# Optimization experiments

Measured on AMD Instinct MI355X. Metric: run time of the kernel, lower is better.

Reference implementation:

```python
import jax, jax.numpy as jnp
import numpy as np

NEURON_CDECAY = 0.5
NEURON_VDECAY = 0.75
NEURON_VTH = 0.5
SPIKE_PSEUDO_GRAD_WINDOW = 0.5

@jax.custom_vjp
def pseudo_spike(v):
    return (v > NEURON_VTH).astype(v.dtype)

def _ps_fwd(v):
    return pseudo_spike(v), v

def _ps_bwd(v, g):
    return (g * (jnp.abs(v - NEURON_VTH) < SPIKE_PSEUDO_GRAD_WINDOW).astype(g.dtype),)

pseudo_spike.defvjp(_ps_fwd, _ps_bwd)

def conv1d(x, w, b):
    # x: (B, Cin, L), w: (Cout, Cin, K), stride 2, VALID padding
    y = jax.lax.conv_general_dilated(x, w, window_strides=(2,), padding='VALID',
                                     dimension_numbers=('NCH', 'OIH', 'NCH'))
    return y + b[None, :, None]

def neuron(syn_out, u, v, s):
    u = u * NEURON_CDECAY + syn_out
    v = v * NEURON_VDECAY * (1.0 - s) + u
    s = pseudo_spike(v)
    return u, v, s

def setup_inputs() -> dict:
    key = jax.random.key(0)
    ks = jax.random.split(key, 18)
    B, T, L = 4096, 50, 360
    h1, h2, h3, A = 256, 256, 128, 2
    def w(k, shape, fan_in):
        bound = 1.0 / np.sqrt(fan_in)
        return jax.random.uniform(k, shape, jnp.float32, -bound, bound)
    return {
        'normal_spikes': (jax.random.uniform(ks[0], (B, 6, T)) < 0.5).astype(jnp.float32),
        'scan_spikes': (jax.random.uniform(ks[1], (B, 1, L, T)) < 0.5).astype(jnp.float32),
        'batch_size': B,
        'conv1_w': w(ks[2], (5, 1, 5), 5),   'conv1_b': w(ks[3], (5,), 5),
        'conv2_w': w(ks[4], (5, 5, 5), 25),  'conv2_b': w(ks[5], (5,), 25),
        'conv3_w': w(ks[6], (5, 5, 5), 25),  'conv3_b': w(ks[7], (5,), 25),
        'fc1_w': w(ks[8], (h1, 216), 216),   'fc1_b': w(ks[9], (h1,), 216),
        'fc2_w': w(ks[10], (h2, h1), h1),    'fc2_b': w(ks[11], (h2,), h1),
        'fc3_w': w(ks[12], (h3, h2), h2),    'fc3_b': w(ks[13], (h3,), h2),
        'fc4_w': w(ks[14], (A, h3), h3),     'fc4_b': w(ks[15], (A,), h3),
    }

def reference(normal_spikes, scan_spikes, batch_size,
              conv1_w, conv1_b, conv2_w, conv2_b, conv3_w, conv3_b,
              fc1_w, fc1_b, fc2_w, fc2_b, fc3_w, fc3_b, fc4_w, fc4_b):
    B = batch_size
    T = normal_spikes.shape[-1]
    A = fc4_w.shape[0]
    # time-major sequences for lax.scan
    scan_seq = jnp.moveaxis(scan_spikes, -1, 0)    # (T, B, 1, 360)
    norm_seq = jnp.moveaxis(normal_spikes, -1, 0)  # (T, B, 6)

    z = lambda *s: jnp.zeros(s, jnp.float32)
    init = (
        (z(B, 5, 178), z(B, 5, 178), z(B, 5, 178)),
        (z(B, 5, 87),  z(B, 5, 87),  z(B, 5, 87)),
        (z(B, 5, 42),  z(B, 5, 42),  z(B, 5, 42)),
        (z(B, 256), z(B, 256), z(B, 256)),
        (z(B, 256), z(B, 256), z(B, 256)),
        (z(B, 128), z(B, 128), z(B, 128)),
        (z(B, A),   z(B, A),   z(B, A)),
        z(B, A),
    )

    def step(carry, xs):
        c1, c2, c3, f1, f2, f3, f4, acc = carry
        scan_x, norm_x = xs
        c1 = neuron(conv1d(scan_x, conv1_w, conv1_b), *c1)
        c2 = neuron(conv1d(c1[2], conv2_w, conv2_b), *c2)
        c3 = neuron(conv1d(c2[2], conv3_w, conv3_b), *c3)
        comb = jnp.concatenate([c3[2].reshape(B, -1), norm_x], axis=1)  # (B, 216)
        f1 = neuron(comb @ fc1_w.T + fc1_b, *f1)
        f2 = neuron(f1[2] @ fc2_w.T + fc2_b, *f2)
        f3 = neuron(f2[2] @ fc3_w.T + fc3_b, *f3)
        f4 = neuron(f3[2] @ fc4_w.T + fc4_b, *f4)
        acc = acc + f4[2]
        return (c1, c2, c3, f1, f2, f3, f4, acc), None

    carry, _ = jax.lax.scan(step, init, (scan_seq, norm_seq))
    return carry[-1] / T
```

## Files before the change

### kernel.cpp

```cpp
#include <hip/hip_runtime.h>
#include <cstdint>
#include <cstddef>


#define NB 4096
#define MTOT (NB * 50)

typedef __attribute__((ext_vector_type(2))) float f32x2;

__device__ __forceinline__ void neuron_update(float syn, float& u, float& v, float& s) {
    u = u * 0.5f + syn;
    v = v * 0.75f * (1.0f - s) + u;
    s = (v > 0.5f) ? 1.0f : 0.0f;
}

__global__ __launch_bounds__(192) void conv1_kernel(
    const float* __restrict__ x, const float* __restrict__ w1,
    const float* __restrict__ b1, unsigned long long* __restrict__ S1)
{
    __shared__ float xl[9000];
    const int tid = threadIdx.x;
    const int b = blockIdx.x;
    const int j = tid;
    const int lbase = (j < 178) ? 2 * j : 354;

    float wr[25], br[5];
#pragma unroll
    for (int q = 0; q < 25; ++q) wr[q] = w1[q];
#pragma unroll
    for (int o = 0; o < 5; ++o) br[o] = b1[o];

    float u[5], v[5], s[5];
#pragma unroll
    for (int o = 0; o < 5; ++o) { u[o] = 0.f; v[o] = 0.f; s[o] = 0.f; }

    const float* xb = x + (size_t)b * 18000;
    for (int half = 0; half < 2; ++half) {
        const int t0 = half * 25;
        __syncthreads();
        for (int e = tid; e < 9000; e += 192)
            xl[e] = xb[(e / 25) * 50 + t0 + (e % 25)];
        __syncthreads();
        for (int dt = 0; dt < 25; ++dt) {
            const int t = t0 + dt;
            float xv[5];
#pragma unroll
            for (int k = 0; k < 5; ++k) xv[k] = xl[(lbase + k) * 25 + dt];
#pragma unroll
            for (int o = 0; o < 5; ++o) {
                float syn = 0.f;
#pragma unroll
                for (int k = 0; k < 5; ++k) syn += wr[o * 5 + k] * xv[k];
                syn += br[o];
                neuron_update(syn, u[o], v[o], s[o]);
                unsigned long long m = __ballot(j < 178 && s[o] > 0.5f);
                if ((tid & 63) == 0)
                    S1[(((size_t)b * 50 + t) * 5 + o) * 3 + (tid >> 6)] = m;
            }
        }
    }
}

__global__ __launch_bounds__(128) void conv2_kernel(
    const unsigned int* __restrict__ S1, const float* __restrict__ w2,
    const float* __restrict__ b2, unsigned int* __restrict__ S2)
{
    __shared__ unsigned int s1l[1501];
    const int tid = threadIdx.x;
    const int b = blockIdx.x;

    float wr[125], br[5];
#pragma unroll
    for (int q = 0; q < 125; ++q) wr[q] = w2[q];
#pragma unroll
    for (int o = 0; o < 5; ++o) br[o] = b2[o];

    const unsigned int* src = S1 + (size_t)b * 1500;
    for (int e = tid; e < 1500; e += 128) s1l[e] = src[e];
    __syncthreads();

    const int p = (tid < 87) ? 2 * tid : 172;
    const int pw = p >> 5, ps = p & 31;

    float u[5], v[5], s[5];
#pragma unroll
    for (int o = 0; o < 5; ++o) { u[o] = 0.f; v[o] = 0.f; s[o] = 0.f; }

    for (int t = 0; t < 50; ++t) {
        float xv[25];
#pragma unroll
        for (int ci = 0; ci < 5; ++ci) {
            const int base = (t * 5 + ci) * 6 + pw;
            unsigned long long bits =
                ((((unsigned long long)s1l[base + 1]) << 32) | (unsigned long long)s1l[base]) >> ps;
#pragma unroll
            for (int k = 0; k < 5; ++k)
                xv[ci * 5 + k] = ((bits >> k) & 1ULL) ? 1.0f : 0.0f;
        }
#pragma unroll
        for (int o = 0; o < 5; ++o) {
            float syn = 0.f;
#pragma unroll
            for (int q = 0; q < 25; ++q) syn += wr[o * 25 + q] * xv[q];
            syn += br[o];
            neuron_update(syn, u[o], v[o], s[o]);
            unsigned long long m = __ballot(tid < 87 && s[o] > 0.5f);
            const size_t outb = (((size_t)b * 50 + t) * 5 + o) * 3;
            if (tid == 0) {
                S2[outb]     = (unsigned int)m;
                S2[outb + 1] = (unsigned int)(m >> 32);
            }
            if (tid == 64) S2[outb + 2] = (unsigned int)m;
        }
    }
}

__global__ __launch_bounds__(64) void conv3_kernel(
    const unsigned int* __restrict__ S2, const float* __restrict__ w3,
    const float* __restrict__ b3, const float* __restrict__ normal,
    unsigned int* __restrict__ ST0)
{
    __shared__ unsigned int s2l[751];
    const int tid = threadIdx.x;
    const int b = blockIdx.x;

    float wr[125], br[5];
#pragma unroll
    for (int q = 0; q < 125; ++q) wr[q] = w3[q];
#pragma unroll
    for (int o = 0; o < 5; ++o) br[o] = b3[o];

    const unsigned int* src = S2 + (size_t)b * 750;
    for (int e = tid; e < 750; e += 64) s2l[e] = src[e];
    __syncthreads();

    const int p = (tid < 42) ? 2 * tid : 82;
    const int pw = p >> 5, ps = p & 31;

    float u[5], v[5], s[5];
#pragma unroll
    for (int o = 0; o < 5; ++o) { u[o] = 0.f; v[o] = 0.f; s[o] = 0.f; }

    for (int t = 0; t < 50; ++t) {
        float xv[25];
#pragma unroll
        for (int ci = 0; ci < 5; ++ci) {
            const int base = (t * 5 + ci) * 3 + pw;
            unsigned long long bits =
                ((((unsigned long long)s2l[base + 1]) << 32) | (unsigned long long)s2l[base]) >> ps;
#pragma unroll
            for (int k = 0; k < 5; ++k)
                xv[ci * 5 + k] = ((bits >> k) & 1ULL) ? 1.0f : 0.0f;
        }
        unsigned long long m[5];
#pragma unroll
        for (int o = 0; o < 5; ++o) {
            float syn = 0.f;
#pragma unroll
            for (int q = 0; q < 25; ++q) syn += wr[o * 25 + q] * xv[q];
            syn += br[o];
            neuron_update(syn, u[o], v[o], s[o]);
            m[o] = __ballot(tid < 42 && s[o] > 0.5f);
        }
        const unsigned long long nm =
            __ballot(tid < 6 && normal[((size_t)b * 6 + tid) * 50 + t] > 0.5f);
        if (tid == 0) {
            const unsigned long long r0 = m[0] | (m[1] << 42);
            const unsigned long long r1 = (m[1] >> 22) | (m[2] << 20) | (m[3] << 62);
            const unsigned long long r2 = (m[3] >> 2) | (m[4] << 40);
            const unsigned long long r3 = (m[4] >> 24) | (nm << 18);
            const size_t mrow = (size_t)b * 50 + t;
            ST0[0 * (size_t)MTOT + mrow] = (unsigned int)r0;
            ST0[1 * (size_t)MTOT + mrow] = (unsigned int)(r0 >> 32);
            ST0[2 * (size_t)MTOT + mrow] = (unsigned int)r1;
            ST0[3 * (size_t)MTOT + mrow] = (unsigned int)(r1 >> 32);
            ST0[4 * (size_t)MTOT + mrow] = (unsigned int)r2;
            ST0[5 * (size_t)MTOT + mrow] = (unsigned int)(r2 >> 32);
            ST0[6 * (size_t)MTOT + mrow] = (unsigned int)r3;
        }
    }
}

__global__ __launch_bounds__(256) void transpose_w_kernel(
    const float* __restrict__ W, float* __restrict__ Wt, int N, int KREAL, int KPAD)
{
    const int idx = blockIdx.x * 256 + threadIdx.x;
    if (idx >= KPAD * N) return;
    const int k = idx / N, n = idx % N;
    Wt[idx] = (k < KREAL) ? W[(size_t)n * KREAL + k] : 0.f;
}

template <int NTOT, int KT>
__global__ __launch_bounds__(256, 2) void pk_gemm_kernel(
    const uint32_t* __restrict__ bitsT,
    const float* __restrict__ Wt,
    const float* __restrict__ bias,
    float* __restrict__ syn,
    int row0)
{
    __shared__ __align__(16) float blds[2][32 * 128];

    const int tid = threadIdx.x;
    const int lane = tid & 63;
    const int wid = tid >> 6;
    const int tm = tid & 15;
    const int tn = tid >> 4;
    const int m0 = blockIdx.x * 256;
    const int nbase = blockIdx.y * 128;

    auto stage = [&](int kt, int buf) {
#pragma unroll
        for (int j = 0; j < 4; ++j) {
            const int c = (j * 4 + wid) * 64 + lane;
            const int row = c >> 5, col = c & 31;
            const float* src = Wt + (size_t)(kt * 32 + row) * NTOT + nbase + col * 4;
            float* dst = &blds[buf][0] + (size_t)(j * 4 + wid) * 256 + lane * 4;
            __builtin_amdgcn_global_load_lds(
                (const __attribute__((address_space(1))) uint32_t*)src,
                (__attribute__((address_space(3))) uint32_t*)dst, 16, 0, 0);
        }
    };

    const int rowA = row0 + m0 + tm * 16;
    auto loadA = [&](int kt, uint4& q0, uint4& q1, uint4& q2, uint4& q3) {
        const uint32_t* p = bitsT + (size_t)kt * MTOT + rowA;
        q0 = *reinterpret_cast<const uint4*>(p);
        q1 = *reinterpret_cast<const uint4*>(p + 4);
        q2 = *reinterpret_cast<const uint4*>(p + 8);
        q3 = *reinterpret_cast<const uint4*>(p + 12);
    };

    uint4 A0, A1, A2, A3, N0, N1, N2, N3;
    loadA(0, A0, A1, A2, A3);
    stage(0, 0);

    f32x2 acc[16][4];
#pragma unroll
    for (int mi = 0; mi < 16; ++mi)
#pragma unroll
        for (int r2 = 0; r2 < 4; ++r2) acc[mi][r2] = (f32x2){0.f, 0.f};

    for (int kt = 0; kt < KT; ++kt) {
        __syncthreads();
        if (kt + 1 < KT) {
            stage(kt + 1, (kt + 1) & 1);
            loadA(kt + 1, N0, N1, N2, N3);
        }

        uint awv[16] = {A0.x, A0.y, A0.z, A0.w, A1.x, A1.y, A1.z, A1.w,
                        A2.x, A2.y, A2.z, A2.w, A3.x, A3.y, A3.z, A3.w};
        const float* bt = &blds[kt & 1][0];

#pragma unroll
        for (int kk = 0; kk < 32; ++kk) {
            f32x2 w2[4];
#pragma unroll
            for (int r2 = 0; r2 < 4; ++r2)
                w2[r2] = *reinterpret_cast<const f32x2*>(bt + kk * 128 + tn * 8 + r2 * 2);
            f32x2 av = {0.f, 0.f};
#pragma unroll
            for (int mi = 0; mi < 16; ++mi) {
                av.x = (float)((awv[mi] >> kk) & 1u);
#pragma unroll
                for (int r2 = 0; r2 < 4; ++r2)
                    asm("v_pk_fma_f32 %0, %1, %2, %0 op_sel_hi:[0,1,1]"
                        : "+v"(acc[mi][r2]) : "v"(av), "v"(w2[r2]));
            }
        }
        if (kt + 1 < KT) { A0 = N0; A1 = N1; A2 = N2; A3 = N3; }
    }

    const int nb = nbase + tn * 8;
    float bsv[8];
#pragma unroll
    for (int q = 0; q < 8; ++q) bsv[q] = bias[nb + q];
#pragma unroll
    for (int mi = 0; mi < 16; ++mi) {
        float* so = syn + (size_t)(m0 + tm * 16 + mi) * NTOT + nb;
        float4 o0, o1;
        o0.x = acc[mi][0].x + bsv[0]; o0.y = acc[mi][0].y + bsv[1];
        o0.z = acc[mi][1].x + bsv[2]; o0.w = acc[mi][1].y + bsv[3];
        o1.x = acc[mi][2].x + bsv[4]; o1.y = acc[mi][2].y + bsv[5];
        o1.z = acc[mi][3].x + bsv[6]; o1.w = acc[mi][3].y + bsv[7];
        *reinterpret_cast<float4*>(so) = o0;
        *reinterpret_cast<float4*>(so + 4) = o1;
    }
}

__global__ __launch_bounds__(256) void fc_scanT_kernel(
    const float* __restrict__ syn, uint32_t* __restrict__ SFT, int b0)
{
    const int tid = threadIdx.x;
    const int lane = tid & 63;
    const int ob = tid >> 6;
    const int bl = blockIdx.x;
    const int o = ob * 64 + lane;

    float u = 0.f, v = 0.f, s = 0.f;
    for (int t = 0; t < 50; ++t) {
        const float sv = syn[((size_t)bl * 50 + t) * 256 + o];
        neuron_update(sv, u, v, s);
        const unsigned long long m = __ballot(s > 0.5f);
        if (lane == 0) {
            const size_t row = (size_t)(b0 + bl) * 50 + t;
            SFT[(size_t)(2 * ob) * MTOT + row]     = (uint32_t)m;
            SFT[(size_t)(2 * ob + 1) * MTOT + row] = (uint32_t)(m >> 32);
        }
    }
}

__global__ __launch_bounds__(256) void fc_scan128_kernel(
    const float* __restrict__ syn, unsigned long long* __restrict__ SF, int b0)
{
    const int tid = threadIdx.x;
    const int wid = blockIdx.x * 4 + (tid >> 6);
    const int lane = tid & 63;
    const int bl = wid >> 1;
    const int ob = wid & 1;
    const int o = ob * 64 + lane;

    float u = 0.f, v = 0.f, s = 0.f;
    for (int t = 0; t < 50; ++t) {
        const float sv = syn[((size_t)bl * 50 + t) * 128 + o];
        neuron_update(sv, u, v, s);
        const unsigned long long m = __ballot(s > 0.5f);
        if (lane == 0) SF[((size_t)(b0 + bl) * 50 + t) * 2 + ob] = m;
    }
}

__global__ __launch_bounds__(256) void fc4_gemm_kernel(
    const unsigned long long* __restrict__ SF3, const float* __restrict__ W,
    const float* __restrict__ bias, float* __restrict__ syn4)
{
    const int m = blockIdx.x * 256 + threadIdx.x;
    const unsigned long long w0 = SF3[(size_t)m * 2];
    const unsigned long long w1 = SF3[(size_t)m * 2 + 1];
    float a0 = 0.f, a1 = 0.f;
#pragma unroll
    for (int i = 0; i < 64; ++i) {
        const float bit = ((w0 >> i) & 1ULL) ? 1.f : 0.f;
        a0 = fmaf(bit, W[i], a0);
        a1 = fmaf(bit, W[128 + i], a1);
    }
#pragma unroll
    for (int i = 0; i < 64; ++i) {
        const float bit = ((w1 >> i) & 1ULL) ? 1.f : 0.f;
        a0 = fmaf(bit, W[64 + i], a0);
        a1 = fmaf(bit, W[192 + i], a1);
    }
    syn4[(size_t)m * 2]     = a0 + bias[0];
    syn4[(size_t)m * 2 + 1] = a1 + bias[1];
}

__global__ __launch_bounds__(64) void fc4_scan_kernel(
    const float* __restrict__ syn4, float* __restrict__ out)
{
    const int b = blockIdx.x * 64 + threadIdx.x;
    float u0 = 0.f, v0 = 0.f, s0 = 0.f, acc0 = 0.f;
    float u1 = 0.f, v1 = 0.f, s1 = 0.f, acc1 = 0.f;
    for (int t = 0; t < 50; ++t) {
        const float x0 = syn4[((size_t)b * 50 + t) * 2];
        const float x1 = syn4[((size_t)b * 50 + t) * 2 + 1];
        neuron_update(x0, u0, v0, s0); acc0 += s0;
        neuron_update(x1, u1, v1, s1); acc1 += s1;
    }
    out[b * 2]     = acc0 / 50.0f;
    out[b * 2 + 1] = acc1 / 50.0f;
}

extern "C" void kernel_launch(void* const* d_in, const int* in_sizes, int n_in,
                              void* d_out, int out_size, void* d_ws, size_t ws_size,
                              hipStream_t stream) {
    (void)in_sizes; (void)n_in; (void)out_size;
    const float* normal = (const float*)d_in[0];
    const float* xscan  = (const float*)d_in[1];
    const float* w1  = (const float*)d_in[3];
    const float* b1  = (const float*)d_in[4];
    const float* w2  = (const float*)d_in[5];
    const float* b2  = (const float*)d_in[6];
    const float* w3  = (const float*)d_in[7];
    const float* b3  = (const float*)d_in[8];
    const float* fw1 = (const float*)d_in[9];
    const float* fb1 = (const float*)d_in[10];
    const float* fw2 = (const float*)d_in[11];
    const float* fb2 = (const float*)d_in[12];
    const float* fw3 = (const float*)d_in[13];
    const float* fb3 = (const float*)d_in[14];
    const float* fw4 = (const float*)d_in[15];
    const float* fb4 = (const float*)d_in[16];
    float* out = (float*)d_out;

    char* wp = (char*)d_ws;
    size_t off = 0;
    auto take = [&](size_t bytes) -> void* {
        void* p = wp + off;
        off += (bytes + 255) & ~(size_t)255;
        return p;
    };
    float* Wt1 = (float*)take((size_t)224 * 256 * 4);
    float* Wt2 = (float*)take((size_t)256 * 256 * 4);
    float* Wt3 = (float*)take((size_t)256 * 128 * 4);
    unsigned long long* S1  = (unsigned long long*)take((size_t)NB * 50 * 15 * 8);
    unsigned int*       S2  = (unsigned int*)take((size_t)NB * 50 * 15 * 4);
    uint32_t* ST0 = (uint32_t*)take((size_t)8 * MTOT * 4);
    uint32_t* ST1 = (uint32_t*)take((size_t)8 * MTOT * 4);
    uint32_t* ST2 = (uint32_t*)take((size_t)8 * MTOT * 4);
    unsigned long long* SF3 = (unsigned long long*)take((size_t)MTOT * 2 * 8);
    float*              syn4 = (float*)take((size_t)MTOT * 2 * 4);

    int chunk = NB;
    while (chunk > 128 && off + (size_t)chunk * 50 * 256 * 4 > ws_size) chunk >>= 1;
    float* syn = (float*)take((size_t)chunk * 50 * 256 * 4);

    transpose_w_kernel<<<(224 * 256 + 255) / 256, 256, 0, stream>>>(fw1, Wt1, 256, 216, 224);
    transpose_w_kernel<<<(256 * 256 + 255) / 256, 256, 0, stream>>>(fw2, Wt2, 256, 256, 256);
    transpose_w_kernel<<<(256 * 128 + 255) / 256, 256, 0, stream>>>(fw3, Wt3, 128, 256, 256);

    conv1_kernel<<<NB, 192, 0, stream>>>(xscan, w1, b1, S1);
    conv2_kernel<<<NB, 128, 0, stream>>>((const unsigned int*)S1, w2, b2, S2);
    conv3_kernel<<<NB, 64, 0, stream>>>(S2, w3, b3, normal, ST0);

    for (int b0 = 0; b0 < NB; b0 += chunk) {
        pk_gemm_kernel<256, 7><<<dim3(chunk * 50 / 256, 2), 256, 0, stream>>>(
            ST0, Wt1, fb1, syn, b0 * 50);
        fc_scanT_kernel<<<chunk, 256, 0, stream>>>(syn, ST1, b0);

        pk_gemm_kernel<256, 8><<<dim3(chunk * 50 / 256, 2), 256, 0, stream>>>(
            ST1, Wt2, fb2, syn, b0 * 50);
        fc_scanT_kernel<<<chunk, 256, 0, stream>>>(syn, ST2, b0);

        pk_gemm_kernel<128, 8><<<dim3(chunk * 50 / 256, 1), 256, 0, stream>>>(
            ST2, Wt3, fb3, syn, b0 * 50);
        fc_scan128_kernel<<<chunk / 2, 256, 0, stream>>>(syn, SF3, b0);
    }

    fc4_gemm_kernel<<<MTOT / 256, 256, 0, stream>>>(SF3, fw4, fb4, syn4);
    fc4_scan_kernel<<<NB / 64, 64, 0, stream>>>(syn4, out);
}
```

Baseline: 1.601 ms.

## Replace packed-FMA bit GEMM with scalar FMA, smaller tile, triple-buffered LDS

Rewrites the bit-spike x weight GEMM used by the three FC layers. Each thread now computes an 8x8 tile with scalar fmaf instead of a 16x8 tile with v_pk_fma_f32, so each block covers 128 rows instead of 256. The kernel asks for 4 blocks per CU instead of 2. Weight tiles move from double to triple buffering in LDS, with explicit s_waitcnt/barrier asm so staging runs two k-steps ahead. The aim is higher occupancy and better latency hiding, at the cost of losing the packed FMA's per-instruction throughput and adding fragile hand-written vmcnt accounting.

```diff
diff --git a/kernel.cpp b/kernel.cpp
--- a/kernel.cpp
+++ b/kernel.cpp
@@ -5,8 +5,6 @@
 
 #define NB 4096
 #define MTOT (NB * 50)
-
-typedef __attribute__((ext_vector_type(2))) float f32x2;
 
 __device__ __forceinline__ void neuron_update(float syn, float& u, float& v, float& s) {
     u = u * 0.5f + syn;
@@ -191,21 +189,21 @@
 }
 
 template <int NTOT, int KT>
-__global__ __launch_bounds__(256, 2) void pk_gemm_kernel(
+__global__ __launch_bounds__(256, 4) void fma_gemm_kernel(
     const uint32_t* __restrict__ bitsT,
     const float* __restrict__ Wt,
     const float* __restrict__ bias,
     float* __restrict__ syn,
     int row0)
 {
-    __shared__ __align__(16) float blds[2][32 * 128];
+    __shared__ __align__(16) float blds[3][32 * 128];
 
     const int tid = threadIdx.x;
     const int lane = tid & 63;
     const int wid = tid >> 6;
     const int tm = tid & 15;
     const int tn = tid >> 4;
-    const int m0 = blockIdx.x * 256;
+    const int m0 = blockIdx.x * 128;
     const int nbase = blockIdx.y * 128;
 
     auto stage = [&](int kt, int buf) {
@@ -221,53 +219,53 @@
         }
     };
 
-    const int rowA = row0 + m0 + tm * 16;
-    auto loadA = [&](int kt, uint4& q0, uint4& q1, uint4& q2, uint4& q3) {
+    const int rowA = row0 + m0 + tm * 8;
+    auto loadA = [&](int kt, uint4& q0, uint4& q1) {
         const uint32_t* p = bitsT + (size_t)kt * MTOT + rowA;
         q0 = *reinterpret_cast<const uint4*>(p);
         q1 = *reinterpret_cast<const uint4*>(p + 4);
-        q2 = *reinterpret_cast<const uint4*>(p + 8);
-        q3 = *reinterpret_cast<const uint4*>(p + 12);
     };
 
-    uint4 A0, A1, A2, A3, N0, N1, N2, N3;
-    loadA(0, A0, A1, A2, A3);
+    uint4 A0, A1, N0, N1;
+    loadA(0, A0, A1);
     stage(0, 0);
-
-    f32x2 acc[16][4];
-#pragma unroll
-    for (int mi = 0; mi < 16; ++mi)
-#pragma unroll
-        for (int r2 = 0; r2 < 4; ++r2) acc[mi][r2] = (f32x2){0.f, 0.f};
-
+    stage(1, 1);
+
+    float acc[8][8];
+#pragma unroll
+    for (int mi = 0; mi < 8; ++mi)
+#pragma unroll
+        for (int r = 0; r < 8; ++r) acc[mi][r] = 0.f;
+
+#pragma unroll 1
     for (int kt = 0; kt < KT; ++kt) {
-        __syncthreads();
-        if (kt + 1 < KT) {
-            stage(kt + 1, (kt + 1) & 1);
-            loadA(kt + 1, N0, N1, N2, N3);
-        }
-
-        uint awv[16] = {A0.x, A0.y, A0.z, A0.w, A1.x, A1.y, A1.z, A1.w,
-                        A2.x, A2.y, A2.z, A2.w, A3.x, A3.y, A3.z, A3.w};
-        const float* bt = &blds[kt & 1][0];
+        if (kt == KT - 1) asm volatile("s_waitcnt vmcnt(0)\ns_barrier" ::: "memory");
+        else              asm volatile("s_waitcnt vmcnt(4)\ns_barrier" ::: "memory");
+
+        if (kt + 1 < KT) loadA(kt + 1, N0, N1);
+        if (kt + 2 < KT) stage(kt + 2, (kt + 2) % 3);
+
+        const uint32_t awv[8] = {A0.x, A0.y, A0.z, A0.w, A1.x, A1.y, A1.z, A1.w};
+        const float* bt = &blds[kt % 3][0];
 
 #pragma unroll
         for (int kk = 0; kk < 32; ++kk) {
-            f32x2 w2[4];
-#pragma unroll
-            for (int r2 = 0; r2 < 4; ++r2)
-                w2[r2] = *reinterpret_cast<const f32x2*>(bt + kk * 128 + tn * 8 + r2 * 2);
-            f32x2 av = {0.f, 0.f};
-#pragma unroll
-            for (int mi = 0; mi < 16; ++mi) {
-                av.x = (float)((awv[mi] >> kk) & 1u);
-#pragma unroll
-                for (int r2 = 0; r2 < 4; ++r2)
-                    asm("v_pk_fma_f32 %0, %1, %2, %0 op_sel_hi:[0,1,1]"
-                        : "+v"(acc[mi][r2]) : "v"(av), "v"(w2[r2]));
+            const float4 b0 = *reinterpret_cast<const float4*>(bt + kk * 128 + tn * 8);
+            const float4 b1 = *reinterpret_cast<const float4*>(bt + kk * 128 + tn * 8 + 4);
+#pragma unroll
+            for (int mi = 0; mi < 8; ++mi) {
+                const float a = (float)((awv[mi] >> kk) & 1u);
+                acc[mi][0] = fmaf(a, b0.x, acc[mi][0]);
+                acc[mi][1] = fmaf(a, b0.y, acc[mi][1]);
+                acc[mi][2] = fmaf(a, b0.z, acc[mi][2]);
+                acc[mi][3] = fmaf(a, b0.w, acc[mi][3]);
+                acc[mi][4] = fmaf(a, b1.x, acc[mi][4]);
+                acc[mi][5] = fmaf(a, b1.y, acc[mi][5]);
+                acc[mi][6] = fmaf(a, b1.z, acc[mi][6]);
+                acc[mi][7] = fmaf(a, b1.w, acc[mi][7]);
             }
         }
-        if (kt + 1 < KT) { A0 = N0; A1 = N1; A2 = N2; A3 = N3; }
+        A0 = N0; A1 = N1;
     }
 
     const int nb = nbase + tn * 8;
@@ -275,13 +273,13 @@
 #pragma unroll
     for (int q = 0; q < 8; ++q) bsv[q] = bias[nb + q];
 #pragma unroll
-    for (int mi = 0; mi < 16; ++mi) {
-        float* so = syn + (size_t)(m0 + tm * 16 + mi) * NTOT + nb;
+    for (int mi = 0; mi < 8; ++mi) {
+        float* so = syn + (size_t)(m0 + tm * 8 + mi) * NTOT + nb;
         float4 o0, o1;
-        o0.x = acc[mi][0].x + bsv[0]; o0.y = acc[mi][0].y + bsv[1];
-        o0.z = acc[mi][1].x + bsv[2]; o0.w = acc[mi][1].y + bsv[3];
-        o1.x = acc[mi][2].x + bsv[4]; o1.y = acc[mi][2].y + bsv[5];
-        o1.z = acc[mi][3].x + bsv[6]; o1.w = acc[mi][3].y + bsv[7];
+        o0.x = acc[mi][0] + bsv[0]; o0.y = acc[mi][1] + bsv[1];
+        o0.z = acc[mi][2] + bsv[2]; o0.w = acc[mi][3] + bsv[3];
+        o1.x = acc[mi][4] + bsv[4]; o1.y = acc[mi][5] + bsv[5];
+        o1.z = acc[mi][6] + bsv[6]; o1.w = acc[mi][7] + bsv[7];
         *reinterpret_cast<float4*>(so) = o0;
         *reinterpret_cast<float4*>(so + 4) = o1;
     }
@@ -421,15 +419,15 @@
     conv3_kernel<<<NB, 64, 0, stream>>>(S2, w3, b3, normal, ST0);
 
     for (int b0 = 0; b0 < NB; b0 += chunk) {
-        pk_gemm_kernel<256, 7><<<dim3(chunk * 50 / 256, 2), 256, 0, stream>>>(
+        fma_gemm_kernel<256, 7><<<dim3(chunk * 50 / 128, 2), 256, 0, stream>>>(
             ST0, Wt1, fb1, syn, b0 * 50);
         fc_scanT_kernel<<<chunk, 256, 0, stream>>>(syn, ST1, b0);
 
-        pk_gemm_kernel<256, 8><<<dim3(chunk * 50 / 256, 2), 256, 0, stream>>>(
+        fma_gemm_kernel<256, 8><<<dim3(chunk * 50 / 128, 2), 256, 0, stream>>>(
             ST1, Wt2, fb2, syn, b0 * 50);
         fc_scanT_kernel<<<chunk, 256, 0, stream>>>(syn, ST2, b0);
 
-        pk_gemm_kernel<128, 8><<<dim3(chunk * 50 / 256, 1), 256, 0, stream>>>(
+        fma_gemm_kernel<128, 8><<<dim3(chunk * 50 / 128, 1), 256, 0, stream>>>(
             ST2, Wt3, fb3, syn, b0 * 50);
         fc_scan128_kernel<<<chunk / 2, 256, 0, stream>>>(syn, SF3, b0);
     }
```

After: 1.814 ms. 13.3% more time.
